# Performance work log

Hardware: AMD Instinct MI355X
Metric: run time of the kernel (lower is better)

## Reference

```python
import jax, jax.numpy as jnp
import numpy as np

NUM_HEADS = 16


def setup_inputs() -> dict:
    key = jax.random.key(0)
    k1, k2, k3, k4 = jax.random.split(key, 4)
    B, N, D = 4, 2048, 1024
    inputs = jax.random.normal(k1, (B, N, D), dtype=jnp.float32)
    w_in = jax.random.normal(k2, (3 * D, D), dtype=jnp.float32) * (D ** -0.5)
    w_out = jax.random.normal(k3, (D, D), dtype=jnp.float32) * (D ** -0.5)
    b_out = jax.random.normal(k4, (D,), dtype=jnp.float32) * 0.02
    return {"inputs": inputs, "w_in": w_in, "w_out": w_out, "b_out": b_out}


def reference(inputs, w_in, w_out, b_out):
    B, N, D = inputs.shape
    H = NUM_HEADS
    Hd = D // H
    # in_proj (torch Linear: x @ W.T), split into Q,K,V
    qkv = jnp.einsum('bnd,ed->bne', inputs, w_in)  # [B,N,3D]
    q, k, v = jnp.split(qkv, 3, axis=-1)
    # [B,H,N,Hd]
    q = q.reshape(B, N, H, Hd).transpose(0, 2, 1, 3)
    k = k.reshape(B, N, H, Hd).transpose(0, 2, 1, 3)
    v = v.reshape(B, N, H, Hd).transpose(0, 2, 1, 3)
    scores = jnp.einsum('bhqd,bhkd->bhqk', q, k) * (Hd ** -0.5)
    causal = jnp.triu(jnp.ones((N, N), dtype=bool), k=1)  # True above diagonal
    scores = jnp.where(causal, -jnp.inf, scores)
    attn = jax.nn.softmax(scores, axis=-1)
    out = jnp.einsum('bhqk,bhkd->bhqd', attn, v)  # [B,H,N,Hd]
    out = out.transpose(0, 2, 1, 3).reshape(B, N, D)
    return jnp.einsum('bnd,ed->bne', out, w_out) + b_out
```

## Files before the change

kernel.cpp:

```cpp
#include <hip/hip_runtime.h>
#include <hip/hip_bf16.h>
#include <cstdint>

typedef __hip_bfloat16 bf16;
typedef short short8 __attribute__((ext_vector_type(8)));
typedef float f32x4 __attribute__((ext_vector_type(4)));

#define AS1C(p) ((const __attribute__((address_space(1))) void*)(p))
#define AS3(p)  ((__attribute__((address_space(3))) void*)(p))

__device__ __forceinline__ float b2f(short s) {
    union { unsigned u; float f; } c; c.u = ((unsigned)(unsigned short)s) << 16; return c.f;
}

template<int CTRL>
__device__ __forceinline__ float dppf(float x) {
    return __int_as_float(__builtin_amdgcn_update_dpp(
        0, __float_as_int(x), CTRL, 0xF, 0xF, true));
}
__device__ __forceinline__ float row_sum16(float x) {
    x += dppf<0xB1>(x);
    x += dppf<0x4E>(x);
    x += dppf<0x141>(x);
    x += dppf<0x140>(x);
    return x;
}

#define N4_X  2097152
#define N4_WI  786432
#define N4_WO  262144
__global__ void cvt_all(const float* __restrict__ x, bf16* __restrict__ xb,
                        const float* __restrict__ wi, bf16* __restrict__ wib,
                        const float* __restrict__ wo, bf16* __restrict__ wob)
{
    int i = blockIdx.x * blockDim.x + threadIdx.x;
    const float* src; bf16* dst; int off;
    if (i < N4_X)                { src = x;  dst = xb;  off = i; }
    else if (i < N4_X + N4_WI)   { src = wi; dst = wib; off = i - N4_X; }
    else                         { src = wo; dst = wob; off = i - N4_X - N4_WI; }
    float4 v = ((const float4*)src)[off];
    __align__(8) bf16 t[4] = { __float2bfloat16(v.x), __float2bfloat16(v.y),
                               __float2bfloat16(v.z), __float2bfloat16(v.w) };
    ((uint2*)dst)[off] = *(const uint2*)t;
}

template<int TM, bool SPLIT_V, bool HAS_BIAS, typename OUT_T>
__global__ __launch_bounds__(TM * 2)
void gemm_bt(const bf16* __restrict__ A, int lda, const bf16* __restrict__ B,
             const float* __restrict__ bias, OUT_T* __restrict__ C, int ldc,
             bf16* __restrict__ vt, int M, int N, int K)
{
    constexpr int NWAVE = TM / 32;
    __shared__ __align__(16) bf16 As[2][TM * 32];
    __shared__ __align__(16) bf16 Bs[2][128 * 32];
    const int tid  = threadIdx.x;
    const int wave = tid >> 6, lane = tid & 63;
    const int wm = wave >> 1, wn = wave & 1;
    const int quad = lane >> 4, l15 = lane & 15;
    const int tile_m = blockIdx.x, tile_n = blockIdx.y;

    const bf16* Ap = A + (size_t)tile_m * TM * lda;
    const bf16* Bp = B + (size_t)tile_n * 128 * K;

    const int srow = lane >> 2;
    const int scol = (lane & 3) * 8;

    f32x4 acc[4][4];
    #pragma unroll
    for (int i = 0; i < 4; i++)
        #pragma unroll
        for (int j = 0; j < 4; j++) acc[i][j] = (f32x4){0.f, 0.f, 0.f, 0.f};

    #define GSTAGE(KI, BUF)                                                        \
        {   const int k0_ = (KI) * 32;                                             \
            _Pragma("unroll")                                                      \
            for (int cc = 0; cc < 2; cc++) {                  \
                int c = wave + cc * NWAVE;                                         \
                const bf16* ga = Ap + (size_t)(c * 16 + srow) * lda + k0_ + scol;  \
                __builtin_amdgcn_global_load_lds(AS1C(ga),                         \
                    AS3(&As[BUF][c * 16 * 32]), 16, 0, 0);                         \
            }                                                                      \
            _Pragma("unroll")                                                      \
            for (int cc = 0; cc < 8 / NWAVE; cc++) {              \
                int c = wave + cc * NWAVE;                                         \
                const bf16* gb = Bp + (size_t)(c * 16 + srow) * K + k0_ + scol;    \
                __builtin_amdgcn_global_load_lds(AS1C(gb),                         \
                    AS3(&Bs[BUF][c * 16 * 32]), 16, 0, 0);                         \
            }                                                                      \
        }

    const int nk = K >> 5;
    GSTAGE(0, 0)
    for (int ki = 0; ki < nk; ki++) {
        __syncthreads();
        const int buf = ki & 1;
        if (ki + 1 < nk) GSTAGE(ki + 1, buf ^ 1)

        short8 af[4], bfr[4];
        #pragma unroll
        for (int mi = 0; mi < 4; mi++)
            af[mi] = *(const short8*)&As[buf][(wm * 64 + mi * 16 + l15) * 32 + quad * 8];
        #pragma unroll
        for (int ni = 0; ni < 4; ni++)
            bfr[ni] = *(const short8*)&Bs[buf][(wn * 64 + ni * 16 + l15) * 32 + quad * 8];
        #pragma unroll
        for (int mi = 0; mi < 4; mi++)
            #pragma unroll
            for (int ni = 0; ni < 4; ni++)
                acc[mi][ni] = __builtin_amdgcn_mfma_f32_16x16x32_bf16(
                    af[mi], bfr[ni], acc[mi][ni], 0, 0, 0);
    }
    #undef GSTAGE

    const bool vtile = SPLIT_V && (tile_n * 128 >= 2048);
    #pragma unroll
    for (int mi = 0; mi < 4; mi++) {
        #pragma unroll
        for (int ni = 0; ni < 4; ni++) {
            int coln = tile_n * 128 + wn * 64 + ni * 16 + l15;
            if (!vtile) {
                float bv = HAS_BIAS ? bias[coln] : 0.f;
                #pragma unroll
                for (int r = 0; r < 4; r++) {
                    int row = tile_m * TM + wm * 64 + mi * 16 + quad * 4 + r;
                    float v = acc[mi][ni][r] + bv;
                    if constexpr (__is_same(OUT_T, float))
                        C[(size_t)row * ldc + coln] = v;
                    else
                        C[(size_t)row * ldc + coln] = __float2bfloat16(v);
                }
            } else {
                int vcol = coln - 2048;
                int row0 = tile_m * TM + wm * 64 + mi * 16 + quad * 4;
                int bb = row0 >> 11, n0 = row0 & 2047;
                __align__(8) bf16 t4[4];
                #pragma unroll
                for (int r = 0; r < 4; r++) t4[r] = __float2bfloat16(acc[mi][ni][r]);
                *(uint2*)&vt[((size_t)(bb * 1024 + vcol)) * 2048 + n0] = *(const uint2*)t4;
            }
        }
    }
}

__global__ __launch_bounds__(256, 3)
void flash_attn(bf16* __restrict__ qkv, const bf16* __restrict__ vt)
{
    const int idx = blockIdx.x;
    const int qt  = 15 - (idx >> 6);
    const int bh  = idx & 63;
    const int b   = bh >> 4, h = bh & 15;
    const int tid = threadIdx.x;
    const int wave = tid >> 6, lane = tid & 63;
    const int quad = lane >> 4, l15 = lane & 15;

    __shared__ __align__(16) bf16 Ks[2][64 * 64];
    __shared__ __align__(16) bf16 Vs[2][64 * 64];
    __shared__ __align__(16) bf16 Ps[4][2][16][72];

    const int q0   = qt * 128;
    const int rowA = wave * 32;
    const size_t rs = 2048;

    const float QSC = 0.18033688011112042f;
    short8 qa[2][2];
    #pragma unroll
    for (int mi = 0; mi < 2; mi++)
        #pragma unroll
        for (int kw = 0; kw < 2; kw++) {
            const bf16* qr = qkv + (size_t)(b * 2048 + q0 + rowA + mi * 16 + l15) * rs
                           + h * 64 + kw * 32 + quad * 8;
            short8 t = *(const short8*)qr;
            #pragma unroll
            for (int e = 0; e < 8; e++)
                t[e] = (short)__bfloat16_as_ushort(__float2bfloat16(b2f(t[e]) * QSC));
            qa[mi][kw] = t;
        }

    f32x4 o[2][4];
    #pragma unroll
    for (int mi = 0; mi < 2; mi++)
        #pragma unroll
        for (int nt = 0; nt < 4; nt++) o[mi][nt] = (f32x4){0.f, 0.f, 0.f, 0.f};
    float lsum[2][4] = {{0.f,0.f,0.f,0.f},{0.f,0.f,0.f,0.f}};

    const bf16* kbase = qkv + (size_t)(b * 2048) * rs + 1024 + h * 64;
    const bf16* vbase = vt + (size_t)(bh * 64) * 2048;

    const int srow8  = lane >> 3;
    const int schunk = (lane & 7) ^ srow8;

    #define STAGE(J, BUF)                                                          \
        {   const int jj = (J);                                                    \
            _Pragma("unroll")                                                      \
            for (int i = 0; i < 2; i++) {                                          \
                int rr_ = wave * 16 + i * 8 + srow8;                               \
                const bf16* gk = kbase + (size_t)(jj * 64 + rr_) * rs + schunk * 8;\
                __builtin_amdgcn_global_load_lds(AS1C(gk),                         \
                    AS3(&Ks[BUF][(wave * 16 + i * 8) * 64]), 16, 0, 0);            \
                const bf16* gv = vbase + (size_t)rr_ * 2048 + jj * 64 + schunk * 8;\
                __builtin_amdgcn_global_load_lds(AS1C(gv),                         \
                    AS3(&Vs[BUF][(wave * 16 + i * 8) * 64]), 16, 0, 0);            \
            }                                                                      \
        }

    STAGE(0, 0)
    const int jmax = 2 * qt + 1;
    for (int j = 0; j <= jmax; j++) {
        __syncthreads();
        const int buf = j & 1;
        if (j < jmax) STAGE(j + 1, buf ^ 1)

        if (j * 64 > q0 + rowA + 31) continue;

        f32x4 s[2][4];
        #pragma unroll
        for (int mi = 0; mi < 2; mi++)
            #pragma unroll
            for (int tc = 0; tc < 4; tc++) s[mi][tc] = (f32x4){0.f,0.f,0.f,0.f};
        #pragma unroll
        for (int kw = 0; kw < 2; kw++) {
            short8 kb[4];
            #pragma unroll
            for (int tc = 0; tc < 4; tc++)
                kb[tc] = *(const short8*)&Ks[buf][(tc * 16 + l15) * 64 +
                         (((kw * 4 + quad) ^ (l15 & 7)) * 8)];
            #pragma unroll
            for (int mi = 0; mi < 2; mi++)
                #pragma unroll
                for (int tc = 0; tc < 4; tc++)
                    s[mi][tc] = __builtin_amdgcn_mfma_f32_16x16x32_bf16(
                        qa[mi][kw], kb[tc], s[mi][tc], 0, 0, 0);
        }
        if (j * 64 + 63 > q0 + rowA) {
            #pragma unroll
            for (int mi = 0; mi < 2; mi++)
                #pragma unroll
                for (int tc = 0; tc < 4; tc++)
                    #pragma unroll
                    for (int rr = 0; rr < 4; rr++)
                        if (j * 64 + tc * 16 + l15 >
                            q0 + rowA + mi * 16 + quad * 4 + rr)
                            s[mi][tc][rr] = -INFINITY;
        }
        #pragma unroll
        for (int mi = 0; mi < 2; mi++) {
            #pragma unroll
            for (int tc = 0; tc < 4; tc++)
                #pragma unroll
                for (int rr = 0; rr < 4; rr++)
                    s[mi][tc][rr] = __builtin_amdgcn_exp2f(s[mi][tc][rr]);
            #pragma unroll
            for (int rr = 0; rr < 4; rr++)
                lsum[mi][rr] += (s[mi][0][rr] + s[mi][1][rr]) +
                                (s[mi][2][rr] + s[mi][3][rr]);
        }
        #pragma unroll
        for (int mi = 0; mi < 2; mi++)
            #pragma unroll
            for (int tc = 0; tc < 4; tc++)
                #pragma unroll
                for (int rr = 0; rr < 4; rr++)
                    Ps[wave][mi][quad * 4 + rr][tc * 16 + l15] =
                        __float2bfloat16(s[mi][tc][rr]);
        #pragma unroll
        for (int kw = 0; kw < 2; kw++) {
            short8 vb[4];
            #pragma unroll
            for (int nt = 0; nt < 4; nt++)
                vb[nt] = *(const short8*)&Vs[buf][(nt * 16 + l15) * 64 +
                         (((kw * 4 + quad) ^ (l15 & 7)) * 8)];
            short8 pa[2];
            #pragma unroll
            for (int mi = 0; mi < 2; mi++)
                pa[mi] = *(const short8*)&Ps[wave][mi][l15][kw * 32 + quad * 8];
            #pragma unroll
            for (int mi = 0; mi < 2; mi++)
                #pragma unroll
                for (int nt = 0; nt < 4; nt++)
                    o[mi][nt] = __builtin_amdgcn_mfma_f32_16x16x32_bf16(
                        pa[mi], vb[nt], o[mi][nt], 0, 0, 0);
        }
    }
    #undef STAGE

    #pragma unroll
    for (int mi = 0; mi < 2; mi++)
        #pragma unroll
        for (int rr = 0; rr < 4; rr++) {
            float inv = 1.f / row_sum16(lsum[mi][rr]);
            int row = b * 2048 + q0 + rowA + mi * 16 + quad * 4 + rr;
            #pragma unroll
            for (int nt = 0; nt < 4; nt++) {
                int col = h * 64 + nt * 16 + l15;
                qkv[(size_t)row * rs + col] = __float2bfloat16(o[mi][nt][rr] * inv);
            }
        }
}

extern "C" void kernel_launch(void* const* d_in, const int* in_sizes, int n_in,
                              void* d_out, int out_size, void* d_ws, size_t ws_size,
                              hipStream_t stream)
{
    const float* x     = (const float*)d_in[0];
    const float* w_in  = (const float*)d_in[1];
    const float* w_out = (const float*)d_in[2];
    const float* b_out = (const float*)d_in[3];
    float* out = (float*)d_out;

    bf16* qkv = (bf16*)d_ws;
    bf16* vt  = qkv + (size_t)8192 * 2048;
    bf16* xb  = vt  + (size_t)4096 * 2048;
    bf16* wib = xb  + (size_t)8192 * 1024;
    bf16* wob = wib + (size_t)3072 * 1024;

    cvt_all<<<(N4_X + N4_WI + N4_WO) / 256, 256, 0, stream>>>(
        x, xb, w_in, wib, w_out, wob);

    gemm_bt<256, true, false, bf16><<<dim3(8192 / 256, 3072 / 128), 512, 0, stream>>>(
        xb, 1024, wib, nullptr, qkv, 2048, vt, 8192, 3072, 1024);
    flash_attn<<<1024, 256, 0, stream>>>(qkv, vt);
    gemm_bt<128, false, true, float><<<dim3(8192 / 128, 1024 / 128), 256, 0, stream>>>(
        qkv, 2048, wob, b_out, out, 1024, nullptr, 8192, 1024, 1024);
}
```

Measured before the change: 242.1 us.

## Use 128x256 GEMM tiles with BK=64 and triple-buffered async LDS pipeline

Replaces the GEMM kernel with a version using 128x256 output tiles, 64-wide k-steps and three LDS buffers, prefetching two stages ahead. It uses explicit vmcnt waits plus a bare barrier. The aim is more MFMA work per barrier and per LDS load, and better hiding of global latency. The large LDS footprint limits occupancy to one block per CU, and the output projection now launches fewer blocks.

Measured after the change: 256.9 us. +6.1%, slower.

```diff
diff --git a/kernel.cpp b/kernel.cpp
--- a/kernel.cpp
+++ b/kernel.cpp
@@ -44,23 +44,22 @@
     ((uint2*)dst)[off] = *(const uint2*)t;
 }
 
-template<int TM, bool SPLIT_V, bool HAS_BIAS, typename OUT_T>
-__global__ __launch_bounds__(TM * 2)
-void gemm_bt(const bf16* __restrict__ A, int lda, const bf16* __restrict__ B,
-             const float* __restrict__ bias, OUT_T* __restrict__ C, int ldc,
-             bf16* __restrict__ vt, int M, int N, int K)
+template<bool SPLIT_V, bool HAS_BIAS, typename OUT_T>
+__global__ __launch_bounds__(512)
+void gemm_bt2(const bf16* __restrict__ A, int lda, const bf16* __restrict__ B,
+              const float* __restrict__ bias, OUT_T* __restrict__ C, int ldc,
+              bf16* __restrict__ vt, int K)
 {
-    constexpr int NWAVE = TM / 32;
-    __shared__ __align__(16) bf16 As[2][TM * 32];
-    __shared__ __align__(16) bf16 Bs[2][128 * 32];
+    __shared__ __align__(16) bf16 As[3][128 * 64];
+    __shared__ __align__(16) bf16 Bs[3][256 * 64];
     const int tid  = threadIdx.x;
     const int wave = tid >> 6, lane = tid & 63;
-    const int wm = wave >> 1, wn = wave & 1;
+    const int wm = wave >> 2, wn = wave & 3;
     const int quad = lane >> 4, l15 = lane & 15;
     const int tile_m = blockIdx.x, tile_n = blockIdx.y;
 
-    const bf16* Ap = A + (size_t)tile_m * TM * lda;
-    const bf16* Bp = B + (size_t)tile_n * 128 * K;
+    const bf16* Ap = A + (size_t)tile_m * 128 * lda;
+    const bf16* Bp = B + (size_t)tile_n * 256 * K;
 
     const int srow = lane >> 2;
     const int scol = (lane & 3) * 8;
@@ -71,58 +70,73 @@
         #pragma unroll
         for (int j = 0; j < 4; j++) acc[i][j] = (f32x4){0.f, 0.f, 0.f, 0.f};
 
-    #define GSTAGE(KI, BUF)                                                        \
-        {   const int k0_ = (KI) * 32;                                             \
+    #define STAGE2(T, BUF)                                                         \
+        {   const int k0_ = (T) * 64;                                              \
             _Pragma("unroll")                                                      \
-            for (int cc = 0; cc < 2; cc++) {                  \
-                int c = wave + cc * NWAVE;                                         \
-                const bf16* ga = Ap + (size_t)(c * 16 + srow) * lda + k0_ + scol;  \
-                __builtin_amdgcn_global_load_lds(AS1C(ga),                         \
-                    AS3(&As[BUF][c * 16 * 32]), 16, 0, 0);                         \
-            }                                                                      \
+            for (int i = 0; i < 2; i++) {                 \
+                const bf16* ga = Ap + (size_t)(wave * 16 + srow) * lda              \
+                               + k0_ + i * 32 + scol;                               \
+                __builtin_amdgcn_global_load_lds(AS1C(ga),                          \
+                    AS3(&As[BUF][(wave * 2 + i) * 512]), 16, 0, 0);                 \
+            }                                                                       \
             _Pragma("unroll")                                                      \
-            for (int cc = 0; cc < 8 / NWAVE; cc++) {              \
-                int c = wave + cc * NWAVE;                                         \
-                const bf16* gb = Bp + (size_t)(c * 16 + srow) * K + k0_ + scol;    \
-                __builtin_amdgcn_global_load_lds(AS1C(gb),                         \
-                    AS3(&Bs[BUF][c * 16 * 32]), 16, 0, 0);                         \
-            }                                                                      \
-        }
-
-    const int nk = K >> 5;
-    GSTAGE(0, 0)
-    for (int ki = 0; ki < nk; ki++) {
-        __syncthreads();
-        const int buf = ki & 1;
-        if (ki + 1 < nk) GSTAGE(ki + 1, buf ^ 1)
-
-        short8 af[4], bfr[4];
+            for (int i = 0; i < 4; i++) {      \
+                const int nc_ = wave * 2 + (i >> 1), kh_ = i & 1;                   \
+                const bf16* gb = Bp + (size_t)(nc_ * 16 + srow) * K                 \
+                               + k0_ + kh_ * 32 + scol;                             \
+                __builtin_amdgcn_global_load_lds(AS1C(gb),                          \
+                    AS3(&Bs[BUF][(wave * 4 + i) * 512]), 16, 0, 0);                 \
+            }                                                                       \
+        }
+
+    const int nk = K >> 6;
+    STAGE2(0, 0)
+    STAGE2(1, 1)
+    int rb = 0, sb = 2;
+    for (int t = 0; t < nk; ++t) {
+        if (t + 1 < nk) asm volatile("s_waitcnt vmcnt(6)" ::: "memory");
+        else            asm volatile("s_waitcnt vmcnt(0)" ::: "memory");
+        __builtin_amdgcn_s_barrier();
+        if (t + 2 < nk) STAGE2(t + 2, sb)
+
+        short8 af[4][2], bfr[4][2];
         #pragma unroll
         for (int mi = 0; mi < 4; mi++)
-            af[mi] = *(const short8*)&As[buf][(wm * 64 + mi * 16 + l15) * 32 + quad * 8];
+            #pragma unroll
+            for (int k = 0; k < 2; k++)
+                af[mi][k] = *(const short8*)
+                    &As[rb][(wm * 4 + mi) * 1024 + k * 512 + l15 * 32 + quad * 8];
         #pragma unroll
         for (int ni = 0; ni < 4; ni++)
-            bfr[ni] = *(const short8*)&Bs[buf][(wn * 64 + ni * 16 + l15) * 32 + quad * 8];
-        #pragma unroll
-        for (int mi = 0; mi < 4; mi++)
-            #pragma unroll
-            for (int ni = 0; ni < 4; ni++)
-                acc[mi][ni] = __builtin_amdgcn_mfma_f32_16x16x32_bf16(
-                    af[mi], bfr[ni], acc[mi][ni], 0, 0, 0);
+            #pragma unroll
+            for (int k = 0; k < 2; k++)
+                bfr[ni][k] = *(const short8*)
+                    &Bs[rb][(wn * 4 + ni) * 1024 + k * 512 + l15 * 32 + quad * 8];
+        #pragma unroll
+        for (int k = 0; k < 2; k++)
+            #pragma unroll
+            for (int mi = 0; mi < 4; mi++)
+                #pragma unroll
+                for (int ni = 0; ni < 4; ni++)
+                    acc[mi][ni] = __builtin_amdgcn_mfma_f32_16x16x32_bf16(
+                        af[mi][k], bfr[ni][k], acc[mi][ni], 0, 0, 0);
+
+        rb = (rb == 2) ? 0 : rb + 1;
+        sb = (sb == 2) ? 0 : sb + 1;
     }
-    #undef GSTAGE
-
-    const bool vtile = SPLIT_V && (tile_n * 128 >= 2048);
+    #undef STAGE2
+
+    const bool vtile = SPLIT_V && (tile_n * 256 >= 2048);
     #pragma unroll
     for (int mi = 0; mi < 4; mi++) {
         #pragma unroll
         for (int ni = 0; ni < 4; ni++) {
-            int coln = tile_n * 128 + wn * 64 + ni * 16 + l15;
+            int coln = tile_n * 256 + wn * 64 + ni * 16 + l15;
             if (!vtile) {
                 float bv = HAS_BIAS ? bias[coln] : 0.f;
                 #pragma unroll
                 for (int r = 0; r < 4; r++) {
-                    int row = tile_m * TM + wm * 64 + mi * 16 + quad * 4 + r;
+                    int row = tile_m * 128 + wm * 64 + mi * 16 + quad * 4 + r;
                     float v = acc[mi][ni][r] + bv;
                     if constexpr (__is_same(OUT_T, float))
                         C[(size_t)row * ldc + coln] = v;
@@ -131,7 +145,7 @@
                 }
             } else {
                 int vcol = coln - 2048;
-                int row0 = tile_m * TM + wm * 64 + mi * 16 + quad * 4;
+                int row0 = tile_m * 128 + wm * 64 + mi * 16 + quad * 4;
                 int bb = row0 >> 11, n0 = row0 & 2047;
                 __align__(8) bf16 t4[4];
                 #pragma unroll
@@ -316,9 +330,9 @@
     cvt_all<<<(N4_X + N4_WI + N4_WO) / 256, 256, 0, stream>>>(
         x, xb, w_in, wib, w_out, wob);
 
-    gemm_bt<256, true, false, bf16><<<dim3(8192 / 256, 3072 / 128), 512, 0, stream>>>(
-        xb, 1024, wib, nullptr, qkv, 2048, vt, 8192, 3072, 1024);
+    gemm_bt2<true, false, bf16><<<dim3(8192 / 128, 3072 / 256), 512, 0, stream>>>(
+        xb, 1024, wib, nullptr, qkv, 2048, vt, 1024);
     flash_attn<<<1024, 256, 0, stream>>>(qkv, vt);
-    gemm_bt<128, false, true, float><<<dim3(8192 / 128, 1024 / 128), 256, 0, stream>>>(
-        qkv, 2048, wob, b_out, out, 1024, nullptr, 8192, 1024, 1024);
-}
+    gemm_bt2<false, true, float><<<dim3(8192 / 128, 1024 / 256), 512, 0, stream>>>(
+        qkv, 2048, wob, b_out, out, 1024, nullptr, 1024);
+}
```

## Replace QKV projection GEMM with 256x256 tile, multi-phase pipelined kernel

Applied to the files above, without the earlier changes.

Adds a new GEMM kernel for the QKV projection that uses 256x256 output tiles with K=64 steps, split into four MFMA phases per step. Each phase interleaves LDS fragment loads, async global-to-LDS prefetch of the next halves, and barriers, and raises wave priority around the MFMA blocks. The goal is to raise arithmetic intensity and overlap memory traffic with compute. In exchange it uses much more LDS and registers, which lowers occupancy, and adds many barriers. The output projection GEMM keeps the old kernel with its V-split path removed.

After: 248.0 us. 1.02x slower.

```diff
diff --git a/kernel.cpp b/kernel.cpp
--- a/kernel.cpp
+++ b/kernel.cpp
@@ -44,11 +44,178 @@
     ((uint2*)dst)[off] = *(const uint2*)t;
 }
 
-template<int TM, bool SPLIT_V, bool HAS_BIAS, typename OUT_T>
+template<bool SPLIT_V, bool HAS_BIAS, typename OUT_T>
+__global__ __launch_bounds__(512, 2)
+void gemm_8ph(const bf16* __restrict__ A, int lda, const bf16* __restrict__ B,
+              const float* __restrict__ bias, OUT_T* __restrict__ C, int ldc,
+              bf16* __restrict__ vt, int K)
+{
+    __shared__ __align__(16) bf16 As[2][2][8192];
+    __shared__ __align__(16) bf16 Bs[2][2][8192];
+    const int tid  = threadIdx.x;
+    const int wave = tid >> 6, lane = tid & 63;
+    const int wm = wave >> 2, wn = wave & 3;
+    const int quad = lane >> 4, l15 = lane & 15;
+    const int tile_m = blockIdx.x, tile_n = blockIdx.y;
+
+    const bf16* Ap = A + (size_t)tile_m * 256 * lda;
+    const bf16* Bp = B + (size_t)tile_n * 256 * K;
+    const int srow = lane >> 2;
+    const int scol = (lane & 3) * 8;
+    const int fo   = l15 * 32 + quad * 8;
+
+    f32x4 acc[2][2][4][2];
+    #pragma unroll
+    for (int a = 0; a < 2; a++)
+        #pragma unroll
+        for (int b = 0; b < 2; b++)
+            #pragma unroll
+            for (int m = 0; m < 4; m++)
+                #pragma unroll
+                for (int n = 0; n < 2; n++) acc[a][b][m][n] = (f32x4){0.f,0.f,0.f,0.f};
+
+    #define STA(T, H)                                                              \
+        {   const int k0_ = (T) * 64, s_ = (T) & 1;                                \
+            _Pragma("unroll")                                                      \
+            for (int i = 0; i < 2; i++) {                                          \
+                int u = wave * 2 + i, c = u >> 1, kh = u & 1;                      \
+                const bf16* g = Ap + (size_t)((H) * 128 + c * 16 + srow) * lda     \
+                              + k0_ + kh * 32 + scol;                              \
+                __builtin_amdgcn_global_load_lds(AS1C(g),                          \
+                    AS3(&As[s_][H][u * 512]), 16, 0, 0);                           \
+            }                                                                      \
+        }
+    #define STB(T, H)                                                              \
+        {   const int k0_ = (T) * 64, s_ = (T) & 1;                                \
+            _Pragma("unroll")                                                      \
+            for (int i = 0; i < 2; i++) {                                          \
+                int u = wave * 2 + i, c = u >> 1, kh = u & 1;                      \
+                const bf16* g = Bp + (size_t)((H) * 128 + c * 16 + srow) * K       \
+                              + k0_ + kh * 32 + scol;                              \
+                __builtin_amdgcn_global_load_lds(AS1C(g),                          \
+                    AS3(&Bs[s_][H][u * 512]), 16, 0, 0);                           \
+            }                                                                      \
+        }
+    #define LGK() { asm volatile("s_waitcnt lgkmcnt(0)" ::: "memory");             \
+                    __builtin_amdgcn_sched_barrier(0); }
+    #define MFMA_PHASE(QM, QN)                                                     \
+        __builtin_amdgcn_s_setprio(1);                                             \
+        _Pragma("unroll")                                                          \
+        for (int kh = 0; kh < 2; kh++)                                             \
+            _Pragma("unroll")                                                      \
+            for (int mi = 0; mi < 4; mi++)                                         \
+                _Pragma("unroll")                                                  \
+                for (int ni = 0; ni < 2; ni++)                                     \
+                    acc[QM][QN][mi][ni] = __builtin_amdgcn_mfma_f32_16x16x32_bf16( \
+                        af[mi][kh], bq[QN][ni][kh], acc[QM][QN][mi][ni], 0, 0, 0); \
+        __builtin_amdgcn_s_setprio(0);
+
+    const int nk = K >> 6;
+    STA(0, 0) STB(0, 0) STA(0, 1) STB(0, 1)
+    STA(1, 0) STB(1, 0)
+    asm volatile("s_waitcnt vmcnt(4)" ::: "memory");
+    __builtin_amdgcn_s_barrier();
+
+    for (int t = 0; t < nk; ++t) {
+        const int s = t & 1;
+        short8 af[4][2];
+        short8 bq[2][2][2];
+
+        #pragma unroll
+        for (int mi = 0; mi < 4; mi++)
+            #pragma unroll
+            for (int kh = 0; kh < 2; kh++)
+                af[mi][kh] = *(const short8*)&As[s][0][((wm*4+mi)*2+kh)*512 + fo];
+        #pragma unroll
+        for (int ni = 0; ni < 2; ni++)
+            #pragma unroll
+            for (int kh = 0; kh < 2; kh++)
+                bq[0][ni][kh] = *(const short8*)&Bs[s][0][((wn*2+ni)*2+kh)*512 + fo];
+        if (t + 1 < nk) STA(t + 1, 1)
+        __builtin_amdgcn_s_barrier();
+        LGK()
+        MFMA_PHASE(0, 0)
+        __builtin_amdgcn_s_barrier();
+
+        #pragma unroll
+        for (int ni = 0; ni < 2; ni++)
+            #pragma unroll
+            for (int kh = 0; kh < 2; kh++)
+                bq[1][ni][kh] = *(const short8*)&Bs[s][1][((wn*2+ni)*2+kh)*512 + fo];
+        if (t + 1 < nk) STB(t + 1, 1)
+        __builtin_amdgcn_s_barrier();
+        LGK()
+        MFMA_PHASE(0, 1)
+        __builtin_amdgcn_s_barrier();
+
+        #pragma unroll
+        for (int mi = 0; mi < 4; mi++)
+            #pragma unroll
+            for (int kh = 0; kh < 2; kh++)
+                af[mi][kh] = *(const short8*)&As[s][1][((wm*4+mi)*2+kh)*512 + fo];
+        if (t + 2 < nk) STA(t + 2, 0)
+        __builtin_amdgcn_s_barrier();
+        LGK()
+        MFMA_PHASE(1, 0)
+        __builtin_amdgcn_s_barrier();
+
+        if (t + 2 < nk) {
+            asm volatile("s_waitcnt vmcnt(2)" ::: "memory");
+            STB(t + 2, 0)
+        } else {
+            asm volatile("s_waitcnt vmcnt(0)" ::: "memory");
+        }
+        __builtin_amdgcn_s_barrier();
+        MFMA_PHASE(1, 1)
+        __builtin_amdgcn_s_barrier();
+    }
+    #undef STA
+    #undef STB
+    #undef LGK
+    #undef MFMA_PHASE
+
+    const bool vtile = SPLIT_V && (tile_n * 256 >= 2048);
+    #pragma unroll
+    for (int qm = 0; qm < 2; qm++) {
+        #pragma unroll
+        for (int qn = 0; qn < 2; qn++) {
+            #pragma unroll
+            for (int mi = 0; mi < 4; mi++) {
+                #pragma unroll
+                for (int ni = 0; ni < 2; ni++) {
+                    int coln = tile_n * 256 + qn * 128 + wn * 32 + ni * 16 + l15;
+                    int row0 = tile_m * 256 + qm * 128 + wm * 64 + mi * 16 + quad * 4;
+                    if (!vtile) {
+                        float bv = HAS_BIAS ? bias[coln] : 0.f;
+                        #pragma unroll
+                        for (int r = 0; r < 4; r++) {
+                            float v = acc[qm][qn][mi][ni][r] + bv;
+                            if constexpr (__is_same(OUT_T, float))
+                                C[(size_t)(row0 + r) * ldc + coln] = v;
+                            else
+                                C[(size_t)(row0 + r) * ldc + coln] = __float2bfloat16(v);
+                        }
+                    } else {
+                        int vcol = coln - 2048;
+                        int bb = row0 >> 11, n0 = row0 & 2047;
+                        __align__(8) bf16 t4[4];
+                        #pragma unroll
+                        for (int r = 0; r < 4; r++)
+                            t4[r] = __float2bfloat16(acc[qm][qn][mi][ni][r]);
+                        *(uint2*)&vt[((size_t)(bb * 1024 + vcol)) * 2048 + n0] =
+                            *(const uint2*)t4;
+                    }
+                }
+            }
+        }
+    }
+}
+
+template<int TM, bool HAS_BIAS, typename OUT_T>
 __global__ __launch_bounds__(TM * 2)
 void gemm_bt(const bf16* __restrict__ A, int lda, const bf16* __restrict__ B,
              const float* __restrict__ bias, OUT_T* __restrict__ C, int ldc,
-             bf16* __restrict__ vt, int M, int N, int K)
+             int K)
 {
     constexpr int NWAVE = TM / 32;
     __shared__ __align__(16) bf16 As[2][TM * 32];
@@ -74,14 +241,14 @@
     #define GSTAGE(KI, BUF)                                                        \
         {   const int k0_ = (KI) * 32;                                             \
             _Pragma("unroll")                                                      \
-            for (int cc = 0; cc < 2; cc++) {                  \
+            for (int cc = 0; cc < 2; cc++) {                                       \
                 int c = wave + cc * NWAVE;                                         \
                 const bf16* ga = Ap + (size_t)(c * 16 + srow) * lda + k0_ + scol;  \
                 __builtin_amdgcn_global_load_lds(AS1C(ga),                         \
                     AS3(&As[BUF][c * 16 * 32]), 16, 0, 0);                         \
             }                                                                      \
             _Pragma("unroll")                                                      \
-            for (int cc = 0; cc < 8 / NWAVE; cc++) {              \
+            for (int cc = 0; cc < 8 / NWAVE; cc++) {                               \
                 int c = wave + cc * NWAVE;                                         \
                 const bf16* gb = Bp + (size_t)(c * 16 + srow) * K + k0_ + scol;    \
                 __builtin_amdgcn_global_load_lds(AS1C(gb),                         \
@@ -112,31 +279,20 @@
     }
     #undef GSTAGE
 
-    const bool vtile = SPLIT_V && (tile_n * 128 >= 2048);
     #pragma unroll
     for (int mi = 0; mi < 4; mi++) {
         #pragma unroll
         for (int ni = 0; ni < 4; ni++) {
             int coln = tile_n * 128 + wn * 64 + ni * 16 + l15;
-            if (!vtile) {
-                float bv = HAS_BIAS ? bias[coln] : 0.f;
-                #pragma unroll
-                for (int r = 0; r < 4; r++) {
-                    int row = tile_m * TM + wm * 64 + mi * 16 + quad * 4 + r;
-                    float v = acc[mi][ni][r] + bv;
-                    if constexpr (__is_same(OUT_T, float))
-                        C[(size_t)row * ldc + coln] = v;
-                    else
-                        C[(size_t)row * ldc + coln] = __float2bfloat16(v);
-                }
-            } else {
-                int vcol = coln - 2048;
-                int row0 = tile_m * TM + wm * 64 + mi * 16 + quad * 4;
-                int bb = row0 >> 11, n0 = row0 & 2047;
-                __align__(8) bf16 t4[4];
-                #pragma unroll
-                for (int r = 0; r < 4; r++) t4[r] = __float2bfloat16(acc[mi][ni][r]);
-                *(uint2*)&vt[((size_t)(bb * 1024 + vcol)) * 2048 + n0] = *(const uint2*)t4;
+            float bv = HAS_BIAS ? bias[coln] : 0.f;
+            #pragma unroll
+            for (int r = 0; r < 4; r++) {
+                int row = tile_m * TM + wm * 64 + mi * 16 + quad * 4 + r;
+                float v = acc[mi][ni][r] + bv;
+                if constexpr (__is_same(OUT_T, float))
+                    C[(size_t)row * ldc + coln] = v;
+                else
+                    C[(size_t)row * ldc + coln] = __float2bfloat16(v);
             }
         }
     }
@@ -316,9 +472,9 @@
     cvt_all<<<(N4_X + N4_WI + N4_WO) / 256, 256, 0, stream>>>(
         x, xb, w_in, wib, w_out, wob);
 
-    gemm_bt<256, true, false, bf16><<<dim3(8192 / 256, 3072 / 128), 512, 0, stream>>>(
-        xb, 1024, wib, nullptr, qkv, 2048, vt, 8192, 3072, 1024);
+    gemm_8ph<true, false, bf16><<<dim3(8192 / 256, 3072 / 256), 512, 0, stream>>>(
+        xb, 1024, wib, nullptr, qkv, 2048, vt, 1024);
     flash_attn<<<1024, 256, 0, stream>>>(qkv, vt);
-    gemm_bt<128, false, true, float><<<dim3(8192 / 128, 1024 / 128), 256, 0, stream>>>(
-        qkv, 2048, wob, b_out, out, 1024, nullptr, 8192, 1024, 1024);
-}
+    gemm_bt<128, true, float><<<dim3(8192 / 128, 1024 / 128), 256, 0, stream>>>(
+        qkv, 2048, wob, b_out, out, 1024, 1024);
+}
```
